# Optimization experiments

Hardware: AMD Instinct MI355X
Metric: run time of the kernel (lower is better)

## Reference

```python
import math
import jax, jax.numpy as jnp
import numpy as np

B, T, C, H = 4, 2048, 1024, 16

def _rope_cos_sin(dim, max_pos):
    half = dim // 2
    pos = jnp.arange(max_pos, dtype=jnp.float32)[:, None]
    freqs = jnp.exp(jnp.arange(half, dtype=jnp.float32) * (-math.log(10000.0) / (half - 1)))[None, :]
    args = pos * freqs  # [T, half]
    return jnp.cos(args), jnp.sin(args)

def _apply_rope(x, cos, sin):
    # x: [B, H, T, D]; pairs (even, odd) along D form complex numbers
    xr = x[..., 0::2]
    xi = x[..., 1::2]
    c = cos[None, None, :, :]
    s = sin[None, None, :, :]
    out_r = xr * c - xi * s
    out_i = xr * s + xi * c
    return jnp.stack([out_r, out_i], axis=-1).reshape(x.shape)

def setup_inputs() -> dict:
    key = jax.random.key(0)
    ks = jax.random.split(key, 9)
    sc = 1.0 / math.sqrt(C)
    return {
        "x": jax.random.normal(ks[0], (B, T, C), jnp.float32),
        "Wq": jax.random.normal(ks[1], (C, C), jnp.float32) * sc,
        "bq": jax.random.normal(ks[2], (C,), jnp.float32) * 0.01,
        "Wk": jax.random.normal(ks[3], (C, C), jnp.float32) * sc,
        "bk": jax.random.normal(ks[4], (C,), jnp.float32) * 0.01,
        "Wv": jax.random.normal(ks[5], (C, C), jnp.float32) * sc,
        "bv": jax.random.normal(ks[6], (C,), jnp.float32) * 0.01,
        "Wp": jax.random.normal(ks[7], (C, C), jnp.float32) * sc,
        "bp": jax.random.normal(ks[8], (C,), jnp.float32) * 0.01,
        "n_head": H,
    }

def reference(x, Wq, bq, Wk, bk, Wv, bv, Wp, bp, n_head):
    Bx, Tx, Cx = x.shape
    D = Cx // n_head
    def heads(w, b):
        return (x @ w + b).reshape(Bx, Tx, n_head, D).transpose(0, 2, 1, 3)  # [B,H,T,D]
    q = heads(Wq, bq)
    k = heads(Wk, bk)
    v = heads(Wv, bv)
    cos, sin = _rope_cos_sin(D, Tx)
    q = _apply_rope(q, cos, sin)
    k = _apply_rope(k, cos, sin)
    att = jnp.einsum("bhtd,bhsd->bhts", q, k) * (1.0 / math.sqrt(D))
    causal = jnp.tril(jnp.ones((Tx, Tx), dtype=bool))
    att = jnp.where(causal[None, None, :, :], att, jnp.float32(-1e10))
    att = jax.nn.softmax(att, axis=-1)
    y = jnp.einsum("bhts,bhsd->bhtd", att, v)
    y = y.transpose(0, 2, 1, 3).reshape(Bx, Tx, Cx)
    return y @ Wp + bp
```

## Files before the change

### kernel.cpp

```cpp
#include <hip/hip_runtime.h>
#include <hip/hip_bf16.h>
#include <stdint.h>

namespace {

constexpr int Bx = 4, Tx = 2048, Cx = 1024, Hx = 16, Dx = 64;
constexpr int Mx = Bx * Tx;

typedef __attribute__((ext_vector_type(8))) short bf16x8;
typedef __attribute__((ext_vector_type(4))) float f32x4;
typedef __attribute__((ext_vector_type(16))) float f32x16;
typedef __attribute__((ext_vector_type(2))) unsigned int u32x2;

__device__ __forceinline__ float b2f(unsigned short u) {
  unsigned int v = ((unsigned int)u) << 16;
  return __builtin_bit_cast(float, v);
}
__device__ __forceinline__ unsigned short f2b(float f) {
  unsigned int v = __builtin_bit_cast(unsigned int, f);
  v += 0x7fffu + ((v >> 16) & 1u);
  return (unsigned short)(v >> 16);
}
__device__ __forceinline__ uint32_t pkbf(float a, float b) {
  __hip_bfloat162 h = __float22bfloat162_rn(float2{a, b});
  uint32_t r;
  __builtin_memcpy(&r, &h, 4);
  return r;
}
__device__ __forceinline__ void pl32swap(uint32_t& a, uint32_t& b) {
  u32x2 r = __builtin_amdgcn_permlane32_swap(a, b, false, false);
  a = r[0];
  b = r[1];
}
__device__ __forceinline__ float xhalf_sum(float x) {
  uint32_t a = __builtin_bit_cast(uint32_t, x), b = a;
  pl32swap(a, b);
  return __builtin_bit_cast(float, a) + __builtin_bit_cast(float, b);
}

#define GLD16(g, lp) __builtin_amdgcn_global_load_lds(                     \
    (__attribute__((address_space(1))) void*)(g),                          \
    (__attribute__((address_space(3))) void*)(lp), 16, 0, 0)

__global__ void ca_cvt(const float* __restrict__ src, unsigned short* __restrict__ dst, int n4) {
  int i = blockIdx.x * blockDim.x + threadIdx.x;
  int stride = gridDim.x * blockDim.x;
  for (; i < n4; i += stride) {
    float4 f = ((const float4*)src)[i];
    ushort4 o;
    o.x = f2b(f.x); o.y = f2b(f.y); o.z = f2b(f.z); o.w = f2b(f.w);
    ((ushort4*)dst)[i] = o;
  }
}

__global__ void ca_wt(const float* __restrict__ W, unsigned short* __restrict__ Wt) {
  __shared__ float tile[32][33];
  int n0 = blockIdx.x * 32, k0 = blockIdx.y * 32;
  int j = threadIdx.x & 31, i = threadIdx.x >> 5;
#pragma unroll
  for (int r = 0; r < 4; ++r)
    tile[i + 8 * r][j] = W[(size_t)(k0 + i + 8 * r) * Cx + n0 + j];
  __syncthreads();
#pragma unroll
  for (int r = 0; r < 4; ++r)
    Wt[(size_t)(n0 + i + 8 * r) * Cx + k0 + j] = f2b(tile[j][i + 8 * r]);
}

__global__ void ca_rtab(float* __restrict__ ct, float* __restrict__ st) {
  int idx = blockIdx.x * blockDim.x + threadIdx.x;
  int t = idx >> 5, i = idx & 31;
  float fr = expf((float)i * -0.29710775393471563f);
  float a = (float)t * fr;
  ct[idx] = cosf(a);
  st[idx] = sinf(a);
}

template <int MODE>
__global__ __launch_bounds__(256) void ca_gemm(
    const unsigned short* __restrict__ A, const unsigned short* __restrict__ Bt,
    const float* __restrict__ b0, const float* __restrict__ b1, const float* __restrict__ b2,
    void* __restrict__ out, int M, int N, int K) {
  __shared__ __align__(16) unsigned short Al[128 * 32];
  __shared__ __align__(16) unsigned short Bl[128 * 32];
  int tid = threadIdx.x;
  int w = tid >> 6, l = tid & 63;
  int m0 = blockIdx.x * 128, n0 = blockIdx.y * 128;
  int wm = (w >> 1) * 64, wn = (w & 1) * 64;
  f32x4 acc[4][4] = {};

  int lr = l & 15, lk8 = (l >> 4) * 8;
  int srow = w * 32 + (l >> 2), scol = (l & 3) * 8;
  const unsigned short* ga0 = A + (size_t)(m0 + srow) * K + scol;
  const unsigned short* gb0 = Bt + (size_t)(n0 + srow) * K + scol;
  unsigned short* la = &Al[w * 1024];
  unsigned short* lb = &Bl[w * 1024];
  int nk = K / 32;
  for (int kt = 0; kt < nk; ++kt) {
    const unsigned short* ga = ga0 + kt * 32;
    const unsigned short* gb = gb0 + kt * 32;
    GLD16(ga, la);
    GLD16(ga + (size_t)16 * K, la + 512);
    GLD16(gb, lb);
    GLD16(gb + (size_t)16 * K, lb + 512);
    __syncthreads();
    bf16x8 af[4], bfr[4];
#pragma unroll
    for (int mi = 0; mi < 4; ++mi) af[mi] = *(const bf16x8*)&Al[(wm + mi * 16 + lr) * 32 + lk8];
#pragma unroll
    for (int ni = 0; ni < 4; ++ni) bfr[ni] = *(const bf16x8*)&Bl[(wn + ni * 16 + lr) * 32 + lk8];
#pragma unroll
    for (int mi = 0; mi < 4; ++mi)
#pragma unroll
      for (int ni = 0; ni < 4; ++ni)
        acc[mi][ni] = __builtin_amdgcn_mfma_f32_16x16x32_bf16(af[mi], bfr[ni], acc[mi][ni], 0, 0, 0);
    __syncthreads();
  }

  int lq4 = (l >> 4) * 4;
  if (MODE == 0) {
    int which = n0 >> 10;
    int nb = n0 & 1023;
    const float* bias = which == 0 ? b0 : (which == 1 ? b1 : b2);
    unsigned short* o = (unsigned short*)out + (size_t)which * M * 1024;
#pragma unroll
    for (int mi = 0; mi < 4; ++mi)
#pragma unroll
      for (int ni = 0; ni < 4; ++ni) {
        int ncol = nb + wn + ni * 16 + lr;
        float bv = bias[ncol];
#pragma unroll
        for (int rg = 0; rg < 4; ++rg) {
          int m = m0 + wm + mi * 16 + lq4 + rg;
          o[(size_t)m * 1024 + ncol] = f2b(acc[mi][ni][rg] + bv);
        }
      }
  } else {
    float* o = (float*)out;
#pragma unroll
    for (int mi = 0; mi < 4; ++mi)
#pragma unroll
      for (int ni = 0; ni < 4; ++ni) {
        int ncol = n0 + wn + ni * 16 + lr;
        float bv = b0[ncol];
#pragma unroll
        for (int rg = 0; rg < 4; ++rg) {
          int m = m0 + wm + mi * 16 + lq4 + rg;
          o[(size_t)m * N + ncol] = acc[mi][ni][rg] + bv;
        }
      }
  }
}

__global__ void ca_rope(unsigned short* __restrict__ q, unsigned short* __restrict__ k,
                        const float* __restrict__ ct, const float* __restrict__ st) {
  constexpr float SC = 0.18033688011112042f;
  int p = blockIdx.x * blockDim.x + threadIdx.x;
  int e = p * 8;
  int col = e & (Cx - 1);
  int t = (e >> 10) & (Tx - 1);
  int j0 = (col & (Dx - 1)) >> 1;
  float c[4], s[4];
#pragma unroll
  for (int jj = 0; jj < 4; ++jj) {
    c[jj] = ct[t * 32 + j0 + jj];
    s[jj] = st[t * 32 + j0 + jj];
  }
  {
    uint4 v = *(uint4*)&q[e];
    unsigned short* u = (unsigned short*)&v;
#pragma unroll
    for (int pr = 0; pr < 4; ++pr) {
      float xr = b2f(u[2 * pr]), xi = b2f(u[2 * pr + 1]);
      u[2 * pr] = f2b((xr * c[pr] - xi * s[pr]) * SC);
      u[2 * pr + 1] = f2b((xr * s[pr] + xi * c[pr]) * SC);
    }
    *(uint4*)&q[e] = v;
  }
  {
    uint4 v = *(uint4*)&k[e];
    unsigned short* u = (unsigned short*)&v;
#pragma unroll
    for (int pr = 0; pr < 4; ++pr) {
      float xr = b2f(u[2 * pr]), xi = b2f(u[2 * pr + 1]);
      u[2 * pr] = f2b(xr * c[pr] - xi * s[pr]);
      u[2 * pr + 1] = f2b(xr * s[pr] + xi * c[pr]);
    }
    *(uint4*)&k[e] = v;
  }
}

__global__ void ca_vt(const unsigned short* __restrict__ v, unsigned short* __restrict__ vT) {
  __shared__ __align__(16) unsigned short tl[64][72];
  int t0 = blockIdx.x * 64;
  int bh = blockIdx.y;
  int b = bh >> 4, h = bh & 15;
  int tid = threadIdx.x;
  const unsigned short* vb = v + (size_t)b * Tx * Cx + h * Dx;
#pragma unroll
  for (int it = 0; it < 2; ++it) {
    int tt = it * 32 + (tid >> 3), d0 = (tid & 7) * 8;
    uint4 x = *(const uint4*)&vb[(size_t)(t0 + tt) * Cx + d0];
    unsigned short* u = (unsigned short*)&x;
#pragma unroll
    for (int jj = 0; jj < 8; ++jj) tl[d0 + jj][tt] = u[jj];
  }
  __syncthreads();
  unsigned short* o = vT + (size_t)bh * Dx * Tx;
#pragma unroll
  for (int it = 0; it < 2; ++it) {
    int d = it * 32 + (tid >> 3), tc = (tid & 7) * 8;
    *(uint4*)&o[(size_t)d * Tx + t0 + tc] = *(const uint4*)&tl[d][tc];
  }
}

__global__ __launch_bounds__(64) void ca_kvfl(
    const unsigned short* __restrict__ k, const unsigned short* __restrict__ vT,
    unsigned short* __restrict__ kfl, unsigned short* __restrict__ vfl) {
  int l = threadIdx.x & 63;
  int bh = blockIdx.x, t = blockIdx.y;
  int b = bh >> 4, h = bh & 15;
  int lo = l & 31, hi = l >> 5;
  const unsigned short* kr = k + (size_t)b * Tx * Cx + h * Dx + (size_t)(t * 32 + lo) * Cx + hi * 8;
  const unsigned short* vr = vT + (size_t)bh * Dx * Tx + (size_t)lo * Tx + t * 32 + hi * 8;
  unsigned short* ko = kfl + ((size_t)bh * 64 + t) * 2048;
  unsigned short* vo = vfl + ((size_t)bh * 64 + t) * 2048;
#pragma unroll
  for (int c = 0; c < 4; ++c) {
    uint4 x = *(const uint4*)(kr + c * 16);
    *(uint4*)(ko + c * 512 + l * 8) = x;
  }
#pragma unroll
  for (int dc = 0; dc < 2; ++dc)
#pragma unroll
    for (int kc = 0; kc < 2; ++kc) {
      uint4 x = *(const uint4*)(vr + (size_t)dc * 32 * Tx + kc * 16);
      *(uint4*)(vo + (dc * 2 + kc) * 512 + l * 8) = x;
    }
}

__global__ __launch_bounds__(64) void ca_attn(
    const unsigned short* __restrict__ q, const unsigned short* __restrict__ kfl,
    const unsigned short* __restrict__ vfl, unsigned short* __restrict__ y) {
  __shared__ uint32_t els[32][33];
  int l = threadIdx.x & 63;
  int bh = blockIdx.x;
  int jp = (int)blockIdx.y;
  int b = bh >> 4, h16 = bh & 15;
  const unsigned short* qp = q + (size_t)b * Tx * Cx + h16 * Dx;
  const unsigned short* kb = kfl + (size_t)bh * 64 * 2048 + l * 8;
  const unsigned short* vb = vfl + (size_t)bh * 64 * 2048 + l * 8;
  int lo = l & 31, hi = l >> 5;
  constexpr float SHIFT = 20.0f;

  for (int pass = 0; pass < 2; ++pass) {
    int qt = pass ? 63 - jp : jp;
    int qbase = qt * 32;

    bf16x8 qf[4];
    {
      const unsigned short* qr = qp + (size_t)(qbase + lo) * Cx + hi * 8;
#pragma unroll
      for (int c = 0; c < 4; ++c) qf[c] = *(const bf16x8*)(qr + c * 16);
    }

    f32x16 acc0 = {}, acc1 = {};
    float lsum = 0.f;
    int nt = qt + 1;

    uint4 rk[4], rv[4];
    auto loadK = [&](int t) {
#pragma unroll
      for (int c = 0; c < 4; ++c) rk[c] = *(const uint4*)(kb + t * 2048 + c * 512);
    };
    auto loadV = [&](int t) {
#pragma unroll
      for (int j = 0; j < 4; ++j) rv[j] = *(const uint4*)(vb + t * 2048 + j * 512);
    };
    loadK(0);
    loadV(0);

    for (int t = 0; t < nt; ++t) {
      bf16x8 kf[4], vf[4];
#pragma unroll
      for (int c = 0; c < 4; ++c) kf[c] = __builtin_bit_cast(bf16x8, rk[c]);
#pragma unroll
      for (int c = 0; c < 4; ++c) vf[c] = __builtin_bit_cast(bf16x8, rv[c]);
      if (t + 1 < nt) { loadK(t + 1); loadV(t + 1); }

      __builtin_amdgcn_s_setprio(1);
      f32x16 sa = {}, sb = {};
      sa = __builtin_amdgcn_mfma_f32_32x32x16_bf16(kf[0], qf[0], sa, 0, 0, 0);
      sb = __builtin_amdgcn_mfma_f32_32x32x16_bf16(kf[1], qf[1], sb, 0, 0, 0);
      sa = __builtin_amdgcn_mfma_f32_32x32x16_bf16(kf[2], qf[2], sa, 0, 0, 0);
      sb = __builtin_amdgcn_mfma_f32_32x32x16_bf16(kf[3], qf[3], sb, 0, 0, 0);
      __builtin_amdgcn_s_setprio(0);

      float p[16];
      if (t == nt - 1) {
#pragma unroll
        for (int r = 0; r < 16; ++r) {
          int kvr = (r & 3) + 8 * (r >> 2) + 4 * hi;
          float tv = sa[r] + sb[r];
          p[r] = (kvr > lo) ? 0.f : exp2f(tv - SHIFT);
        }
      } else {
#pragma unroll
        for (int r = 0; r < 16; ++r) p[r] = exp2f((sa[r] + sb[r]) - SHIFT);
      }
      float sm[8];
#pragma unroll
      for (int r = 0; r < 8; ++r) sm[r] = p[2 * r] + p[2 * r + 1];
#pragma unroll
      for (int r = 0; r < 4; ++r) sm[r] = sm[2 * r] + sm[2 * r + 1];
      float ps = (sm[0] + sm[1]) + (sm[2] + sm[3]);
      lsum += xhalf_sum(ps);

      uint32_t pk[8];
#pragma unroll
      for (int i = 0; i < 8; ++i) pk[i] = pkbf(p[2 * i], p[2 * i + 1]);
      pl32swap(pk[0], pk[2]);
      pl32swap(pk[1], pk[3]);
      pl32swap(pk[4], pk[6]);
      pl32swap(pk[5], pk[7]);
      uint4 xw{pk[0], pk[1], pk[2], pk[3]}, yw{pk[4], pk[5], pk[6], pk[7]};
      bf16x8 PB0 = __builtin_bit_cast(bf16x8, xw);
      bf16x8 PB1 = __builtin_bit_cast(bf16x8, yw);
      __builtin_amdgcn_s_setprio(1);
      acc0 = __builtin_amdgcn_mfma_f32_32x32x16_bf16(vf[0], PB0, acc0, 0, 0, 0);
      acc1 = __builtin_amdgcn_mfma_f32_32x32x16_bf16(vf[2], PB0, acc1, 0, 0, 0);
      acc0 = __builtin_amdgcn_mfma_f32_32x32x16_bf16(vf[1], PB1, acc0, 0, 0, 0);
      acc1 = __builtin_amdgcn_mfma_f32_32x32x16_bf16(vf[3], PB1, acc1, 0, 0, 0);
      __builtin_amdgcn_s_setprio(0);
    }

    float rl = __builtin_amdgcn_rcpf(lsum);
#pragma unroll
    for (int dc = 0; dc < 2; ++dc) {
      f32x16 a = dc ? acc1 : acc0;
#pragma unroll
      for (int i = 0; i < 8; ++i) {
        uint32_t pkd = pkbf(a[2 * i] * rl, a[2 * i + 1] * rl);
        int d2 = (i & 1) + 4 * (i >> 1) + 2 * hi + dc * 16;
        els[lo][d2] = pkd;
      }
    }
    __syncthreads();
    unsigned short* yp = y + (size_t)b * Tx * Cx + h16 * Dx;
#pragma unroll
    for (int pp = 0; pp < 16; ++pp) {
      int qr = 2 * pp + hi;
      uint32_t val = els[qr][lo];
      *(uint32_t*)(yp + (size_t)(qbase + qr) * Cx + lo * 2) = val;
    }
    __syncthreads();
  }
}

}

extern "C" void kernel_launch(void* const* d_in, const int* in_sizes, int n_in,
                              void* d_out, int out_size, void* d_ws, size_t ws_size,
                              hipStream_t stream) {
  const float* x = (const float*)d_in[0];
  const float* Wq = (const float*)d_in[1];
  const float* bq = (const float*)d_in[2];
  const float* Wk = (const float*)d_in[3];
  const float* bk = (const float*)d_in[4];
  const float* Wv = (const float*)d_in[5];
  const float* bv = (const float*)d_in[6];
  const float* Wp = (const float*)d_in[7];
  const float* bp = (const float*)d_in[8];

  unsigned short* xb = (unsigned short*)d_ws;
  unsigned short* wt = xb + (size_t)Mx * Cx;
  float* ct = (float*)(wt + (size_t)4 * Cx * Cx);
  float* st = ct + Tx * 32;
  unsigned short* qb = (unsigned short*)(st + Tx * 32);
  unsigned short* kb = qb + (size_t)Mx * Cx;
  unsigned short* vb = kb + (size_t)Mx * Cx;
  unsigned short* vT = vb + (size_t)Mx * Cx;
  unsigned short* yb = vT + (size_t)Mx * Cx;
  unsigned short* kfl = yb + (size_t)Mx * Cx;
  unsigned short* vfl = kfl + (size_t)64 * 64 * 2048;

  ca_cvt<<<dim3(2048), dim3(256), 0, stream>>>(x, xb, Mx * Cx / 4);
  ca_wt<<<dim3(32, 32), dim3(256), 0, stream>>>(Wq, wt + (size_t)0 * Cx * Cx);
  ca_wt<<<dim3(32, 32), dim3(256), 0, stream>>>(Wk, wt + (size_t)1 * Cx * Cx);
  ca_wt<<<dim3(32, 32), dim3(256), 0, stream>>>(Wv, wt + (size_t)2 * Cx * Cx);
  ca_wt<<<dim3(32, 32), dim3(256), 0, stream>>>(Wp, wt + (size_t)3 * Cx * Cx);
  ca_rtab<<<dim3(Tx * 32 / 256), dim3(256), 0, stream>>>(ct, st);

  ca_gemm<0><<<dim3(64, 24), dim3(256), 0, stream>>>(xb, wt, bq, bk, bv, qb, Mx, 3072, Cx);
  ca_rope<<<dim3(Mx * Cx / 8 / 256), dim3(256), 0, stream>>>(qb, kb, ct, st);
  ca_vt<<<dim3(Tx / 64, Bx * Hx), dim3(256), 0, stream>>>(vb, vT);
  ca_kvfl<<<dim3(64, 64), dim3(64), 0, stream>>>(kb, vT, kfl, vfl);
  ca_attn<<<dim3(64, 32), dim3(64), 0, stream>>>(qb, kfl, vfl, yb);
  ca_gemm<1><<<dim3(64, 8), dim3(256), 0, stream>>>(yb, wt + (size_t)3 * Cx * Cx, bp,
                                                    nullptr, nullptr, d_out, Mx, Cx, Cx);
}
```

Measured before the change: 245.8 us.

## Fuse RoPE into QKV GEMM epilogue and compute softmax sums via MFMA

Applies the rotary embedding and the query scale inside the QKV GEMM epilogue, using a lane shuffle to fetch the paired element, and removes the separate RoPE kernel along with its read and write of Q and K. In attention, the QK score MFMAs now accumulate into a single register tile instead of two, and the row sums of P come from an extra MFMA against a ones vector instead of VALU adds plus a permlane reduction. This trades two extra MFMAs per tile and a longer dependency chain on the score accumulator for fewer VALU operations, and the GEMM epilogue gains per-element table loads.

```diff
diff --git a/kernel.cpp b/kernel.cpp
--- a/kernel.cpp
+++ b/kernel.cpp
@@ -31,11 +31,6 @@
   u32x2 r = __builtin_amdgcn_permlane32_swap(a, b, false, false);
   a = r[0];
   b = r[1];
-}
-__device__ __forceinline__ float xhalf_sum(float x) {
-  uint32_t a = __builtin_bit_cast(uint32_t, x), b = a;
-  pl32swap(a, b);
-  return __builtin_bit_cast(float, a) + __builtin_bit_cast(float, b);
 }
 
 #define GLD16(g, lp) __builtin_amdgcn_global_load_lds(                     \
@@ -79,6 +74,7 @@
 __global__ __launch_bounds__(256) void ca_gemm(
     const unsigned short* __restrict__ A, const unsigned short* __restrict__ Bt,
     const float* __restrict__ b0, const float* __restrict__ b1, const float* __restrict__ b2,
+    const float* __restrict__ ctab, const float* __restrict__ stab,
     void* __restrict__ out, int M, int N, int K) {
   __shared__ __align__(16) unsigned short Al[128 * 32];
   __shared__ __align__(16) unsigned short Bl[128 * 32];
@@ -118,20 +114,33 @@
 
   int lq4 = (l >> 4) * 4;
   if (MODE == 0) {
+    constexpr float SC = 0.18033688011112042f;
     int which = n0 >> 10;
     int nb = n0 & 1023;
     const float* bias = which == 0 ? b0 : (which == 1 ? b1 : b2);
     unsigned short* o = (unsigned short*)out + (size_t)which * M * 1024;
+    bool doRope = which < 2;
+    float scl = which == 0 ? SC : 1.0f;
 #pragma unroll
     for (int mi = 0; mi < 4; ++mi)
 #pragma unroll
       for (int ni = 0; ni < 4; ++ni) {
         int ncol = nb + wn + ni * 16 + lr;
         float bv = bias[ncol];
+        int j = (ncol & 63) >> 1;
+        bool even = (ncol & 1) == 0;
 #pragma unroll
         for (int rg = 0; rg < 4; ++rg) {
           int m = m0 + wm + mi * 16 + lq4 + rg;
-          o[(size_t)m * 1024 + ncol] = f2b(acc[mi][ni][rg] + bv);
+          float val = acc[mi][ni][rg] + bv;
+          if (doRope) {
+            int t = m & (Tx - 1);
+            float c = ctab[t * 32 + j], s = stab[t * 32 + j];
+            float other = __shfl_xor(val, 1);
+            float res = even ? (val * c - other * s) : (other * s + val * c);
+            val = res * scl;
+          }
+          o[(size_t)m * 1024 + ncol] = f2b(val);
         }
       }
   } else {
@@ -148,44 +157,6 @@
           o[(size_t)m * N + ncol] = acc[mi][ni][rg] + bv;
         }
       }
-  }
-}
-
-__global__ void ca_rope(unsigned short* __restrict__ q, unsigned short* __restrict__ k,
-                        const float* __restrict__ ct, const float* __restrict__ st) {
-  constexpr float SC = 0.18033688011112042f;
-  int p = blockIdx.x * blockDim.x + threadIdx.x;
-  int e = p * 8;
-  int col = e & (Cx - 1);
-  int t = (e >> 10) & (Tx - 1);
-  int j0 = (col & (Dx - 1)) >> 1;
-  float c[4], s[4];
-#pragma unroll
-  for (int jj = 0; jj < 4; ++jj) {
-    c[jj] = ct[t * 32 + j0 + jj];
-    s[jj] = st[t * 32 + j0 + jj];
-  }
-  {
-    uint4 v = *(uint4*)&q[e];
-    unsigned short* u = (unsigned short*)&v;
-#pragma unroll
-    for (int pr = 0; pr < 4; ++pr) {
-      float xr = b2f(u[2 * pr]), xi = b2f(u[2 * pr + 1]);
-      u[2 * pr] = f2b((xr * c[pr] - xi * s[pr]) * SC);
-      u[2 * pr + 1] = f2b((xr * s[pr] + xi * c[pr]) * SC);
-    }
-    *(uint4*)&q[e] = v;
-  }
-  {
-    uint4 v = *(uint4*)&k[e];
-    unsigned short* u = (unsigned short*)&v;
-#pragma unroll
-    for (int pr = 0; pr < 4; ++pr) {
-      float xr = b2f(u[2 * pr]), xi = b2f(u[2 * pr + 1]);
-      u[2 * pr] = f2b(xr * c[pr] - xi * s[pr]);
-      u[2 * pr + 1] = f2b(xr * s[pr] + xi * c[pr]);
-    }
-    *(uint4*)&k[e] = v;
   }
 }
 
@@ -251,6 +222,9 @@
   const unsigned short* vb = vfl + (size_t)bh * 64 * 2048 + l * 8;
   int lo = l & 31, hi = l >> 5;
   constexpr float SHIFT = 20.0f;
+  const uint32_t one2 = 0x3F803F80u;
+  uint4 onesw{one2, one2, one2, one2};
+  bf16x8 ONES = __builtin_bit_cast(bf16x8, onesw);
 
   for (int pass = 0; pass < 2; ++pass) {
     int qt = pass ? 63 - jp : jp;
@@ -263,8 +237,7 @@
       for (int c = 0; c < 4; ++c) qf[c] = *(const bf16x8*)(qr + c * 16);
     }
 
-    f32x16 acc0 = {}, acc1 = {};
-    float lsum = 0.f;
+    f32x16 acc0 = {}, acc1 = {}, sacc = {};
     int nt = qt + 1;
 
     uint4 rk[4], rv[4];
@@ -288,11 +261,11 @@
       if (t + 1 < nt) { loadK(t + 1); loadV(t + 1); }
 
       __builtin_amdgcn_s_setprio(1);
-      f32x16 sa = {}, sb = {};
-      sa = __builtin_amdgcn_mfma_f32_32x32x16_bf16(kf[0], qf[0], sa, 0, 0, 0);
-      sb = __builtin_amdgcn_mfma_f32_32x32x16_bf16(kf[1], qf[1], sb, 0, 0, 0);
-      sa = __builtin_amdgcn_mfma_f32_32x32x16_bf16(kf[2], qf[2], sa, 0, 0, 0);
-      sb = __builtin_amdgcn_mfma_f32_32x32x16_bf16(kf[3], qf[3], sb, 0, 0, 0);
+      f32x16 s = {};
+      s = __builtin_amdgcn_mfma_f32_32x32x16_bf16(kf[0], qf[0], s, 0, 0, 0);
+      s = __builtin_amdgcn_mfma_f32_32x32x16_bf16(kf[1], qf[1], s, 0, 0, 0);
+      s = __builtin_amdgcn_mfma_f32_32x32x16_bf16(kf[2], qf[2], s, 0, 0, 0);
+      s = __builtin_amdgcn_mfma_f32_32x32x16_bf16(kf[3], qf[3], s, 0, 0, 0);
       __builtin_amdgcn_s_setprio(0);
 
       float p[16];
@@ -300,20 +273,12 @@
 #pragma unroll
         for (int r = 0; r < 16; ++r) {
           int kvr = (r & 3) + 8 * (r >> 2) + 4 * hi;
-          float tv = sa[r] + sb[r];
-          p[r] = (kvr > lo) ? 0.f : exp2f(tv - SHIFT);
+          p[r] = (kvr > lo) ? 0.f : exp2f(s[r] - SHIFT);
         }
       } else {
 #pragma unroll
-        for (int r = 0; r < 16; ++r) p[r] = exp2f((sa[r] + sb[r]) - SHIFT);
+        for (int r = 0; r < 16; ++r) p[r] = exp2f(s[r] - SHIFT);
       }
-      float sm[8];
-#pragma unroll
-      for (int r = 0; r < 8; ++r) sm[r] = p[2 * r] + p[2 * r + 1];
-#pragma unroll
-      for (int r = 0; r < 4; ++r) sm[r] = sm[2 * r] + sm[2 * r + 1];
-      float ps = (sm[0] + sm[1]) + (sm[2] + sm[3]);
-      lsum += xhalf_sum(ps);
 
       uint32_t pk[8];
 #pragma unroll
@@ -328,12 +293,14 @@
       __builtin_amdgcn_s_setprio(1);
       acc0 = __builtin_amdgcn_mfma_f32_32x32x16_bf16(vf[0], PB0, acc0, 0, 0, 0);
       acc1 = __builtin_amdgcn_mfma_f32_32x32x16_bf16(vf[2], PB0, acc1, 0, 0, 0);
+      sacc = __builtin_amdgcn_mfma_f32_32x32x16_bf16(ONES, PB0, sacc, 0, 0, 0);
       acc0 = __builtin_amdgcn_mfma_f32_32x32x16_bf16(vf[1], PB1, acc0, 0, 0, 0);
       acc1 = __builtin_amdgcn_mfma_f32_32x32x16_bf16(vf[3], PB1, acc1, 0, 0, 0);
+      sacc = __builtin_amdgcn_mfma_f32_32x32x16_bf16(ONES, PB1, sacc, 0, 0, 0);
       __builtin_amdgcn_s_setprio(0);
     }
 
-    float rl = __builtin_amdgcn_rcpf(lsum);
+    float rl = __builtin_amdgcn_rcpf(sacc[0]);
 #pragma unroll
     for (int dc = 0; dc < 2; ++dc) {
       f32x16 a = dc ? acc1 : acc0;
@@ -390,11 +357,11 @@
   ca_wt<<<dim3(32, 32), dim3(256), 0, stream>>>(Wp, wt + (size_t)3 * Cx * Cx);
   ca_rtab<<<dim3(Tx * 32 / 256), dim3(256), 0, stream>>>(ct, st);
 
-  ca_gemm<0><<<dim3(64, 24), dim3(256), 0, stream>>>(xb, wt, bq, bk, bv, qb, Mx, 3072, Cx);
-  ca_rope<<<dim3(Mx * Cx / 8 / 256), dim3(256), 0, stream>>>(qb, kb, ct, st);
+  ca_gemm<0><<<dim3(64, 24), dim3(256), 0, stream>>>(xb, wt, bq, bk, bv, ct, st, qb, Mx, 3072, Cx);
   ca_vt<<<dim3(Tx / 64, Bx * Hx), dim3(256), 0, stream>>>(vb, vT);
   ca_kvfl<<<dim3(64, 64), dim3(64), 0, stream>>>(kb, vT, kfl, vfl);
   ca_attn<<<dim3(64, 32), dim3(64), 0, stream>>>(qb, kfl, vfl, yb);
   ca_gemm<1><<<dim3(64, 8), dim3(256), 0, stream>>>(yb, wt + (size_t)3 * Cx * Cx, bp,
-                                                    nullptr, nullptr, d_out, Mx, Cx, Cx);
-}
+                                                    nullptr, nullptr, nullptr, nullptr,
+                                                    d_out, Mx, Cx, Cx);
+}
```

Result: faster. 236.5 us (-3.8%).
